# Kernel optimization log

Hardware: AMD Instinct MI355X
Metric: run time of the kernel (lower is better)

## Reference

```python
import jax, jax.numpy as jnp
import numpy as np

# Tensor layout: x is [b, c, d, h, w, p, q, r] = [batch, channels, D, H, W, pd, ph, pw]
LETTERS = 'bcdhwpqr'

def axial_linear(x, W, b, axis, S, C):
    """LinearAlongDims1 over dims [1, axis]: jointly mixes channels and one
    spatial/patch axis. Torch flattens in (spatial, channel) order, so the
    (S*C, S*C) weight is reshaped to [S_out, C_out, S_in, C_in]."""
    a = LETTERS[axis]
    W4 = W.reshape(S, C, S, C)
    out_sub = LETTERS.replace('c', 'Y').replace(a, 'X')
    y = jnp.einsum(f'{LETTERS},XY{a}c->{out_sub}', x, W4)
    bshape = [1] * 8
    bshape[1] = C
    bshape[axis] = S
    return y + b.reshape(S, C).T.reshape(bshape)


def _make_linear_params(key, n):
    kw, kb = jax.random.split(key)
    bound = 1.0 / np.sqrt(n)
    W = jax.random.uniform(kw, (n, n), jnp.float32, -bound, bound)
    b = jax.random.uniform(kb, (n,), jnp.float32, -bound, bound)
    return W, b


def setup_inputs() -> dict:
    key = jax.random.key(0)
    ks = jax.random.split(key, 7)
    B, C, D, P = 2, 64, 16, 4
    x = jax.random.normal(ks[0], (B, C, D, D, D, P, P, P), jnp.float32)
    w_d, b_d = _make_linear_params(ks[1], C * D)      # image_d: dims [1,2]
    w_h, b_h = _make_linear_params(ks[2], C * D)      # image_h: dims [1,3]
    w_w, b_w = _make_linear_params(ks[3], C * D)      # image_w: dims [1,4]
    w_pd, b_pd = _make_linear_params(ks[4], C * P)    # patch_d: dims [1,5]
    w_ph, b_ph = _make_linear_params(ks[5], C * P)    # patch_h: dims [1,6]
    w_pw, b_pw = _make_linear_params(ks[6], C * P)    # patch_w: dims [1,7]
    return {
        'x': x,
        'w_d': w_d, 'b_d': b_d, 'w_h': w_h, 'b_h': b_h, 'w_w': w_w, 'b_w': b_w,
        'w_pd': w_pd, 'b_pd': b_pd, 'w_ph': w_ph, 'b_ph': b_ph,
        'w_pw': w_pw, 'b_pw': b_pw,
    }


def reference(x, w_d, b_d, w_h, b_h, w_w, b_w,
              w_pd, b_pd, w_ph, b_ph, w_pw, b_pw):
    C = x.shape[1]
    D = x.shape[2]
    P = x.shape[5]
    y = axial_linear(x, w_pd, b_pd, 5, P, C)
    y = y + axial_linear(x, w_ph, b_ph, 6, P, C)
    y = y + axial_linear(x, w_pw, b_pw, 7, P, C)
    y = y + axial_linear(x, w_d, b_d, 2, D, C)
    y = y + axial_linear(x, w_h, b_h, 3, D, C)
    y = y + axial_linear(x, w_w, b_w, 4, D, C)
    # shapes match -> leaky_relu + residual (module returns y; gn(x) is discarded)
    y = x + jax.nn.leaky_relu(y, negative_slope=0.01)
    return y
```

## Files before the change

### kernel.cpp

```cpp
#include <hip/hip_runtime.h>

typedef __attribute__((ext_vector_type(8))) short short8;
typedef __attribute__((ext_vector_type(4))) float floatx4;


__device__ __forceinline__ unsigned short f2bf(float f){
  unsigned int u = __float_as_uint(f);
  u += 0x7FFFu + ((u >> 16) & 1u);
  return (unsigned short)(u >> 16);
}

template<int AX>
__device__ __forceinline__ int tidx(int m, int a, int c){
  if      (AX==0){ int b=m>>14, t=m&16383;                         return (b<<24)|(c<<18)|(a<<14)|t; }
  else if (AX==1){ int b=m>>14, d=(m>>10)&15, t=m&1023;            return (b<<24)|(c<<18)|(d<<14)|(a<<10)|t; }
  else           { int b=m>>14, d=(m>>10)&15, h=(m>>6)&15, t=m&63; return (b<<24)|(c<<18)|(d<<14)|(h<<10)|(a<<6)|t; }
}

template<int AX>
__device__ __forceinline__ int srcbase(int m){
  if      (AX==0) return ((m>>14)<<24) | (((m>>10)&15)<<16) | (((m>>6)&15)<<12) | ((m&63)<<6);
  else if (AX==1) return ((m>>14)<<24) | (((m>>10)&15)<<20) | (((m>>6)&15)<<12) | ((m&63)<<6);
  else            return ((m>>14)<<24) | (((m>>10)&15)<<20) | (((m>>6)&15)<<16) | ((m&63)<<6);
}

#define ASYNC_CP16(g, l) \
  __builtin_amdgcn_global_load_lds( \
      (const __attribute__((address_space(1))) unsigned int*)(g), \
      (__attribute__((address_space(3))) unsigned int*)(l), 16, 0, 0)

__global__ __launch_bounds__(256) void castw_all(
    const float* __restrict__ wa, const float* __restrict__ wb, const float* __restrict__ wc,
    const float* __restrict__ wd_, const float* __restrict__ we, const float* __restrict__ wf,
    const float* __restrict__ bd_, const float* __restrict__ bh_, const float* __restrict__ bw_,
    const float* __restrict__ bpd_, const float* __restrict__ bph_, const float* __restrict__ bpw_,
    unsigned short* oa, unsigned short* ob, unsigned short* oc,
    unsigned short* od, unsigned short* oe, unsigned short* of_,
    float* __restrict__ Bimg, float* __restrict__ Bpat){
  int blk = blockIdx.x;
  if (blk < 6528){
    const float* src; unsigned short* dst; int idx;
    if (blk < 6144){ int wsel = blk >> 11, loc = blk & 2047;
      src = wsel==0?wa:(wsel==1?wb:wc); dst = wsel==0?oa:(wsel==1?ob:oc);
      idx = loc*256 + threadIdx.x; }
    else { int b2 = blk - 6144, wsel = b2 >> 7, loc = b2 & 127;
      src = wsel==0?wd_:(wsel==1?we:wf); dst = wsel==0?od:(wsel==1?oe:of_);
      idx = loc*256 + threadIdx.x; }
    float2 v = ((const float2*)src)[idx];
    ((unsigned int*)dst)[idx] = (unsigned int)f2bf(v.x) | ((unsigned int)f2bf(v.y) << 16);
  } else if (blk < 7552){
    int idx = (blk - 6528)*256 + threadIdx.x;
    int c = idx & 63, wv = (idx>>6)&15, hv = (idx>>10)&15, dv = idx>>14;
    Bimg[idx] = bd_[dv*64+c] + bh_[hv*64+c] + bw_[wv*64+c];
  } else {
    int idx = (blk - 7552)*256 + threadIdx.x;
    int c = idx & 63, tt = idx>>6;
    int p = tt>>4, q = (tt>>2)&3, r = tt&3;
    Bpat[idx] = bpd_[p*64+c] + bph_[q*64+c] + bpw_[r*64+c];
  }
}

__global__ __launch_bounds__(256) void transpose_cx(const float* __restrict__ x,
                                                    unsigned short* __restrict__ xt){
  __shared__ float T[64][65];
  int b  = blockIdx.x >> 12;
  int s0 = (blockIdx.x & 4095) * 64;
  int t = threadIdx.x;
  int cr = t >> 4, sq = t & 15;
  #pragma unroll
  for (int it = 0; it < 4; it++){
    int c = it*16 + cr;
    float4 v = *(const float4*)(x + (b<<24) + (c<<18) + s0 + sq*4);
    T[c][sq*4+0]=v.x; T[c][sq*4+1]=v.y; T[c][sq*4+2]=v.z; T[c][sq*4+3]=v.w;
  }
  __syncthreads();
  int sw = t >> 2, cq = t & 3;
  unsigned int pk[8];
  #pragma unroll
  for (int i=0;i<8;i++){
    float f0 = T[cq*16 + 2*i    ][sw];
    float f1 = T[cq*16 + 2*i + 1][sw];
    pk[i] = (unsigned int)f2bf(f0) | ((unsigned int)f2bf(f1) << 16);
  }
  uint4* dst = (uint4*)(xt + (b<<24) + ((s0 + sw)<<6) + cq*16);
  dst[0] = make_uint4(pk[0],pk[1],pk[2],pk[3]);
  dst[1] = make_uint4(pk[4],pk[5],pk[6],pk[7]);
}

template<int AXI, bool FIRST>
__device__ __forceinline__ void patch_axis(const unsigned short* Xs,
                                           const unsigned short* __restrict__ W,
                                           float* AccL, int w, int l16, int q8){
  floatx4 acc[4][2];
  #pragma unroll
  for (int nt=0;nt<4;nt++)
    #pragma unroll
    for (int mt=0;mt<2;mt++) acc[nt][mt] = (floatx4){0.f,0.f,0.f,0.f};

  #pragma unroll 2
  for (int kit = 0; kit < 8; kit++){
    int a = kit >> 1;
    short8 bf[2], af[4];
    int u = (AXI==0) ? (a*16 + l16)
          : (AXI==1) ? ((l16>>2)*16 + a*4 + (l16&3))
                     : ((l16>>2)*16 + (l16&3)*4 + a);
    int jg = ((kit & 1) << 2) + q8;
    #pragma unroll
    for (int mt = 0; mt < 2; mt++){
      int r = mt*64 + u;
      int j = jg ^ ((r ^ (r >> 3)) & 7);
      bf[mt] = *(const short8*)(Xs + r*64 + j*8);
    }
    #pragma unroll
    for (int nt = 0; nt < 4; nt++){
      int n = w*64 + nt*16 + l16;
      af[nt] = *(const short8*)(W + n*256 + kit*32 + q8*8);
    }
    #pragma unroll
    for (int nt=0; nt<4; nt++)
      #pragma unroll
      for (int mt=0; mt<2; mt++)
        acc[nt][mt] = __builtin_amdgcn_mfma_f32_16x16x32_bf16(af[nt], bf[mt], acc[nt][mt], 0,0,0);
  }

  int uo = (AXI==0) ? (w*16 + l16)
         : (AXI==1) ? ((l16>>2)*16 + w*4 + (l16&3))
                    : ((l16>>2)*16 + (l16&3)*4 + w);
  #pragma unroll
  for (int nt=0; nt<4; nt++)
    #pragma unroll
    for (int mt=0; mt<2; mt++){
      float* p = AccL + (mt*64 + uo)*65 + nt*16 + q8*4;
      #pragma unroll
      for (int rg=0; rg<4; rg++){
        if (FIRST) p[rg]  = acc[nt][mt][rg];
        else       p[rg] += acc[nt][mt][rg];
      }
    }
}

__global__ __launch_bounds__(256) void patch_fused(const unsigned short* __restrict__ xt,
    const unsigned short* __restrict__ Wp_, const unsigned short* __restrict__ Wq_,
    const unsigned short* __restrict__ Wr_, float* __restrict__ out){
  __shared__ float AccL[2*64*65];
  __shared__ unsigned short Xs[8192];
  int pp = blockIdx.x;
  int b = pp >> 11, dpair = pp & 2047;
  const unsigned short* xp = xt + (b<<24) + dpair*8192;
  int t = threadIdx.x, w = t>>6, lane = t&63, q8 = lane>>4, l16 = lane&15;

  #pragma unroll
  for (int i = 0; i < 4; i++){
    int L = i*256 + t;
    int r = L >> 3, jl = L & 7;
    int jg = jl ^ ((r ^ (r >> 3)) & 7);
    ASYNC_CP16(xp + r*64 + jg*8, Xs + i*2048 + w*512);
  }
  __syncthreads();

  patch_axis<0,true >(Xs, Wp_, AccL, w, l16, q8);
  __syncthreads();
  patch_axis<1,false>(Xs, Wq_, AccL, w, l16, q8);
  __syncthreads();
  patch_axis<2,false>(Xs, Wr_, AccL, w, l16, q8);
  __syncthreads();

  int sbase = dpair*128;
  #pragma unroll
  for (int it = 0; it < 32; it++){
    int lin = it*256 + t;
    int c = lin >> 7, rem = lin & 127, pt = rem >> 6, u = rem & 63;
    out[(b<<24) | (c<<18) | (sbase + pt*64 + u)] = AccL[(pt*64+u)*65 + c];
  }
}

template<int AX, int EPI>
__global__ __launch_bounds__(256) void gemm_img(const unsigned short* __restrict__ xt,
                                                const unsigned short* __restrict__ Wbf,
                                                float* __restrict__ out,
                                                const float* __restrict__ x,
                                                const float* __restrict__ Bimg,
                                                const float* __restrict__ Bpat){
  constexpr int K  = 1024;
  constexpr int SA = (AX==0)?(1<<20):(AX==1)?(1<<16):(1<<12);
  int B = blockIdx.x;
  int xcd = B & 7, seq = B >> 3;
  int nt = seq & 7;
  int mt = (seq >> 3) * 8 + xcd;

  __shared__ unsigned short Xs[2][4096];
  __shared__ unsigned short Ws[2][4096];

  int t = threadIdx.x, lane = t & 63, wid = t >> 6;
  int wn = (wid & 1) << 6, wm = (wid >> 1) << 6;
  int q = lane >> 4, l16 = lane & 15;

  floatx4 acc[4][4];
  #pragma unroll
  for (int i=0;i<4;i++)
    #pragma unroll
    for (int j=0;j<4;j++) acc[i][j] = (floatx4){0.f,0.f,0.f,0.f};

  const unsigned short* Wp = Wbf + (size_t)nt*128*K;

  int row = t >> 2;
  int jj  = (t & 3) ^ ((t >> 3) & 3);
  int base0 = srcbase<AX>(mt*128 + row);
  int base1 = srcbase<AX>(mt*128 + 64 + row);
  const unsigned short* wg0 = Wp + row*K + jj*8;
  const unsigned short* wg1 = Wp + (row+64)*K + jj*8;

  int xoff[4], woff[4];
  #pragma unroll
  for (int i=0;i<4;i++){
    int rx = wm + i*16 + l16; xoff[i] = rx*32 + ((q ^ ((rx>>1)&3))<<3);
    int rw = wn + i*16 + l16; woff[i] = rw*32 + ((q ^ ((rw>>1)&3))<<3);
  }

  #define STAGE_T(k0, s) do { \
    int aK_ = (k0) >> 6; \
    int cc_ = ((k0) & 63) + jj*8; \
    ASYNC_CP16(xt + base0 + aK_*SA + cc_, &Xs[s][wid*512]); \
    ASYNC_CP16(xt + base1 + aK_*SA + cc_, &Xs[s][2048 + wid*512]); \
    ASYNC_CP16(wg0 + (k0), &Ws[s][wid*512]); \
    ASYNC_CP16(wg1 + (k0), &Ws[s][2048 + wid*512]); \
  } while(0)

  STAGE_T(0, 0);
  __syncthreads();

  for (int k0 = 0; k0 < K; k0 += 32){
    int cur = (k0 >> 5) & 1;
    if (k0 + 32 < K) STAGE_T(k0 + 32, cur ^ 1);

    short8 wf[4], xf[4];
    #pragma unroll
    for (int i=0;i<4;i++){
      wf[i] = *(const short8*)&Ws[cur][woff[i]];
      xf[i] = *(const short8*)&Xs[cur][xoff[i]];
    }
    #pragma unroll
    for (int i=0;i<4;i++)
      #pragma unroll
      for (int j=0;j<4;j++)
        acc[i][j] = __builtin_amdgcn_mfma_f32_16x16x32_bf16(wf[i], xf[j], acc[i][j], 0,0,0);

    __syncthreads();
  }
  #undef STAGE_T

  #pragma unroll
  for (int i=0;i<4;i++){
    #pragma unroll
    for (int j=0;j<4;j++){
      int mg = mt*128 + wm + j*16 + l16;
      if (EPI){
        int d = (mg>>10)&15, h = (mg>>6)&15, tt = mg&63;
        int n0 = nt*128 + wn + i*16 + q*4;
        int a = n0 >> 6, c0 = n0 & 63;
        float4 bi = *(const float4*)(Bimg + (((d*16 + h)*16 + a)*64 + c0));
        float4 bp = *(const float4*)(Bpat + (tt*64 + c0));
        float bs0 = bi.x + bp.x, bs1 = bi.y + bp.y, bs2 = bi.z + bp.z, bs3 = bi.w + bp.w;
        #pragma unroll
        for (int rg=0; rg<4; rg++){
          int ng = n0 + rg;
          int idx = tidx<AX>(mg, ng>>6, ng&63);
          float bsum = (rg==0)?bs0:(rg==1)?bs1:(rg==2)?bs2:bs3;
          float y = out[idx] + acc[i][j][rg] + bsum;
          out[idx] = x[idx] + (y >= 0.f ? y : 0.01f*y);
        }
      } else {
        #pragma unroll
        for (int rg=0; rg<4; rg++){
          int ng = nt*128 + wn + i*16 + q*4 + rg;
          int idx = tidx<AX>(mg, ng>>6, ng&63);
          out[idx] += acc[i][j][rg];
        }
      }
    }
  }
}

extern "C" void kernel_launch(void* const* d_in, const int* in_sizes, int n_in,
                              void* d_out, int out_size, void* d_ws, size_t ws_size,
                              hipStream_t stream){
  const float* x = (const float*)d_in[0];
  const float* Wsrc[6] = {(const float*)d_in[1], (const float*)d_in[3], (const float*)d_in[5],
                          (const float*)d_in[7], (const float*)d_in[9], (const float*)d_in[11]};
  const float* Bsrc[6] = {(const float*)d_in[2], (const float*)d_in[4], (const float*)d_in[6],
                          (const float*)d_in[8], (const float*)d_in[10], (const float*)d_in[12]};
  float* out = (float*)d_out;
  char* ws = (char*)d_ws;

  const size_t welems[6] = {1024u*1024u, 1024u*1024u, 1024u*1024u,
                            256u*256u, 256u*256u, 256u*256u};
  size_t wOff[6], o = 0;
  for (int i=0;i<6;i++){ wOff[i] = o; o += welems[i]*2; }
  size_t xtOff = (o + 255) & ~(size_t)255;
  size_t bimgOff = xtOff + ((size_t)1u<<25)*2;
  size_t bpatOff = bimgOff + (size_t)16*16*16*64*4;
  unsigned short* xt = (unsigned short*)(ws + xtOff);
  float* Bimg = (float*)(ws + bimgOff);
  float* Bpat = (float*)(ws + bpatOff);
  unsigned short* Wbf[6];
  for (int i=0;i<6;i++) Wbf[i] = (unsigned short*)(ws + wOff[i]);

  castw_all<<<7616,256,0,stream>>>(Wsrc[0],Wsrc[1],Wsrc[2],Wsrc[3],Wsrc[4],Wsrc[5],
                                   Bsrc[0],Bsrc[1],Bsrc[2],Bsrc[3],Bsrc[4],Bsrc[5],
                                   Wbf[0],Wbf[1],Wbf[2],Wbf[3],Wbf[4],Wbf[5],
                                   Bimg, Bpat);
  transpose_cx<<<8192,256,0,stream>>>(x, xt);

  patch_fused<<<4096,256,0,stream>>>(xt, Wbf[3], Wbf[4], Wbf[5], out);

  gemm_img<0,0><<<2048,256,0,stream>>>(xt, Wbf[0], out, nullptr, nullptr, nullptr);
  gemm_img<1,0><<<2048,256,0,stream>>>(xt, Wbf[1], out, nullptr, nullptr, nullptr);
  gemm_img<2,1><<<2048,256,0,stream>>>(xt, Wbf[2], out, x, Bimg, Bpat);
}
```

Measured before the change: 933.0 us.

## Use single-buffered 64-wide K tiles in image-axis GEMM instead of double buffering

The image-axis GEMM loop now loads a full 64-element K slice (one spatial index a) per iteration into a single LDS buffer, with an 8-way XOR swizzle, and runs two MFMA sub-steps per slice. The previous version double-buffered 32-wide slices. The change halves the number of loop iterations and barriers and makes each global load cover a contiguous 128-byte channel run. In exchange it gives up overlap between the async copy and the MFMA compute, since every slice waits on a barrier before its compute starts.

```diff
diff --git a/kernel.cpp b/kernel.cpp
--- a/kernel.cpp
+++ b/kernel.cpp
@@ -188,12 +188,12 @@
   int nt = seq & 7;
   int mt = (seq >> 3) * 8 + xcd;
 
-  __shared__ unsigned short Xs[2][4096];
-  __shared__ unsigned short Ws[2][4096];
+  __shared__ unsigned short Xs[128*64];
+  __shared__ unsigned short Ws[128*64];
 
   int t = threadIdx.x, lane = t & 63, wid = t >> 6;
   int wn = (wid & 1) << 6, wm = (wid >> 1) << 6;
-  int q = lane >> 4, l16 = lane & 15;
+  int q8 = lane >> 4, l16 = lane & 15;
 
   floatx4 acc[4][4];
   #pragma unroll
@@ -203,51 +203,47 @@
 
   const unsigned short* Wp = Wbf + (size_t)nt*128*K;
 
-  int row = t >> 2;
-  int jj  = (t & 3) ^ ((t >> 3) & 3);
-  int base0 = srcbase<AX>(mt*128 + row);
-  int base1 = srcbase<AX>(mt*128 + 64 + row);
-  const unsigned short* wg0 = Wp + row*K + jj*8;
-  const unsigned short* wg1 = Wp + (row+64)*K + jj*8;
+  int rr = t >> 3;
+  int jg = (t & 7) ^ ((t >> 3) & 7);
+  int baseX[4], baseWo[4];
+  #pragma unroll
+  for (int c=0;c<4;c++){
+    int r = c*32 + rr;
+    baseX[c]  = srcbase<AX>(mt*128 + r) + jg*8;
+    baseWo[c] = r*K + jg*8;
+  }
 
   int xoff[4], woff[4];
   #pragma unroll
   for (int i=0;i<4;i++){
-    int rx = wm + i*16 + l16; xoff[i] = rx*32 + ((q ^ ((rx>>1)&3))<<3);
-    int rw = wn + i*16 + l16; woff[i] = rw*32 + ((q ^ ((rw>>1)&3))<<3);
-  }
-
-  #define STAGE_T(k0, s) do { \
-    int aK_ = (k0) >> 6; \
-    int cc_ = ((k0) & 63) + jj*8; \
-    ASYNC_CP16(xt + base0 + aK_*SA + cc_, &Xs[s][wid*512]); \
-    ASYNC_CP16(xt + base1 + aK_*SA + cc_, &Xs[s][2048 + wid*512]); \
-    ASYNC_CP16(wg0 + (k0), &Ws[s][wid*512]); \
-    ASYNC_CP16(wg1 + (k0), &Ws[s][2048 + wid*512]); \
-  } while(0)
-
-  STAGE_T(0, 0);
-  __syncthreads();
-
-  for (int k0 = 0; k0 < K; k0 += 32){
-    int cur = (k0 >> 5) & 1;
-    if (k0 + 32 < K) STAGE_T(k0 + 32, cur ^ 1);
-
-    short8 wf[4], xf[4];
-    #pragma unroll
-    for (int i=0;i<4;i++){
-      wf[i] = *(const short8*)&Ws[cur][woff[i]];
-      xf[i] = *(const short8*)&Xs[cur][xoff[i]];
-    }
-    #pragma unroll
-    for (int i=0;i<4;i++)
+    int rx = wm + i*16 + l16; xoff[i] = rx*64 + ((q8 ^ (rx & 7)) << 3);
+    int rw = wn + i*16 + l16; woff[i] = rw*64 + ((q8 ^ (rw & 7)) << 3);
+  }
+
+  for (int a = 0; a < 16; a++){
+    #pragma unroll
+    for (int c=0;c<4;c++){
+      ASYNC_CP16(xt + baseX[c] + a*SA, Xs + c*2048 + wid*512);
+      ASYNC_CP16(Wp + baseWo[c] + a*64, Ws + c*2048 + wid*512);
+    }
+    __syncthreads();
+
+    #pragma unroll
+    for (int kk=0; kk<2; kk++){
+      short8 wf[4], xf[4];
       #pragma unroll
-      for (int j=0;j<4;j++)
-        acc[i][j] = __builtin_amdgcn_mfma_f32_16x16x32_bf16(wf[i], xf[j], acc[i][j], 0,0,0);
-
+      for (int i=0;i<4;i++){
+        wf[i] = *(const short8*)&Ws[woff[i] ^ (kk<<5)];
+        xf[i] = *(const short8*)&Xs[xoff[i] ^ (kk<<5)];
+      }
+      #pragma unroll
+      for (int i=0;i<4;i++)
+        #pragma unroll
+        for (int j=0;j<4;j++)
+          acc[i][j] = __builtin_amdgcn_mfma_f32_16x16x32_bf16(wf[i], xf[j], acc[i][j], 0,0,0);
+    }
     __syncthreads();
   }
-  #undef STAGE_T
 
   #pragma unroll
   for (int i=0;i<4;i++){
@@ -256,7 +252,7 @@
       int mg = mt*128 + wm + j*16 + l16;
       if (EPI){
         int d = (mg>>10)&15, h = (mg>>6)&15, tt = mg&63;
-        int n0 = nt*128 + wn + i*16 + q*4;
+        int n0 = nt*128 + wn + i*16 + q8*4;
         int a = n0 >> 6, c0 = n0 & 63;
         float4 bi = *(const float4*)(Bimg + (((d*16 + h)*16 + a)*64 + c0));
         float4 bp = *(const float4*)(Bpat + (tt*64 + c0));
@@ -272,7 +268,7 @@
       } else {
         #pragma unroll
         for (int rg=0; rg<4; rg++){
-          int ng = nt*128 + wn + i*16 + q*4 + rg;
+          int ng = nt*128 + wn + i*16 + q8*4 + rg;
           int idx = tidx<AX>(mg, ng>>6, ng&63);
           out[idx] += acc[i][j][rg];
         }
```

Result: faster. 852.7 us (-8.6%).
